# Kernel tuning notes

Measured on AMD Instinct MI355X. Metric: run time of the kernel, lower is better.

The kernel has to match this reference:

```python
import jax, jax.numpy as jnp
import numpy as np

B, S, D, H, HD = 4, 2048, 1024, 16, 64
R, L = 4, 256
MASKED_BIAS = -10000.0


def setup_inputs() -> dict:
    key = jax.random.key(0)
    ks = jax.random.split(key, 8)
    w = 0.02  # GPT-2 style init scale keeps softmax logits sane
    return {
        "hidden_states": jax.random.normal(ks[0], (B, S, D), jnp.float32),
        "latent": jax.random.normal(ks[1], (B, L), jnp.float32),
        "c_attn_w": jax.random.normal(ks[2], (D, 3 * D), jnp.float32) * w,
        "c_attn_b": jnp.zeros((3 * D,), jnp.float32),
        "c_proj_w": jax.random.normal(ks[3], (D, D), jnp.float32) * w,
        "c_proj_b": jnp.zeros((D,), jnp.float32),
        "text_w": jax.random.normal(ks[4], (R, D + 1, D), jnp.float32) * w,
        "text_b": jnp.zeros((R, D), jnp.float32),
        "lat_w": jax.random.normal(ks[5], (R, L + 1, D), jnp.float32) * w,
        "lat_b": jnp.zeros((R, D), jnp.float32),
    }


def _lmf(v, latent, text_w, text_b, lat_w, lat_b):
    # append bias-1 column, apply rank-R linears, sum over rank, outer-fuse
    b, s, _ = v.shape
    v1 = jnp.concatenate([v, jnp.ones((b, s, 1), v.dtype)], axis=-1)          # [B,S,D+1]
    l1 = jnp.concatenate([latent, jnp.ones((b, 1), latent.dtype)], axis=-1)   # [B,L+1]
    text_fusion = jnp.einsum("bsi,rio->bso", v1, text_w) + text_b.sum(0)      # [B,S,D]
    latent_fusion = jnp.einsum("bi,rio->bo", l1, lat_w) + lat_b.sum(0)        # [B,D]
    return text_fusion * latent_fusion[:, None, :]


def reference(hidden_states, latent, c_attn_w, c_attn_b, c_proj_w, c_proj_b,
              text_w, text_b, lat_w, lat_b):
    qkv = hidden_states @ c_attn_w + c_attn_b                # [B,S,3D] (Conv1D)
    q, k, v = jnp.split(qkv, 3, axis=-1)
    v = _lmf(v, latent, text_w, text_b, lat_w, lat_b)        # LMF on value stream

    def split_heads(t):
        return t.reshape(B, S, H, HD).transpose(0, 2, 1, 3)  # [B,H,S,HD]

    q, k, v = split_heads(q), split_heads(k), split_heads(v)
    scores = jnp.einsum("bhqd,bhkd->bhqk", q, k) / jnp.asarray(HD, q.dtype) ** 0.5
    causal = jnp.tril(jnp.ones((S, S), bool))                # use_causal_mask=True
    scores = jnp.where(causal, scores, jnp.asarray(MASKED_BIAS, scores.dtype))
    probs = jax.nn.softmax(scores, axis=-1)                  # attn_pdrop=0 (eval)
    attn = jnp.einsum("bhqk,bhkd->bhqd", probs, v)
    attn = attn.transpose(0, 2, 1, 3).reshape(B, S, D)       # merge heads
    return attn @ c_proj_w + c_proj_b                        # resid_pdrop=0 (eval)
```

## Files before the change

kernel.cpp:

```cpp
#include <hip/hip_runtime.h>
#include <hip/hip_bf16.h>

typedef __bf16 bf16;
typedef __bf16 bf16x8 __attribute__((ext_vector_type(8)));
typedef float f32x4 __attribute__((ext_vector_type(4)));
typedef unsigned short u16;
typedef unsigned int u32;

__device__ __forceinline__ u16 f2bf_bits(float f) {
    union { float f; u32 u; } v;
    v.f = f;
    u32 r = v.u + 0x7FFFu + ((v.u >> 16) & 1u);
    return (u16)(r >> 16);
}

__device__ __forceinline__ u32 pack_bf2(float a, float b) {
    union { __bf16 h[2]; u32 u; } v;
    v.h[0] = (__bf16)a;
    v.h[1] = (__bf16)b;
    return v.u;
}

__device__ __forceinline__ void gload_lds16(const void* g, void* l) {
    __builtin_amdgcn_global_load_lds((const __attribute__((address_space(1))) void*)g,
                                     (__attribute__((address_space(3))) void*)l, 16, 0, 0);
}


__global__ __launch_bounds__(256) void cvt_bf16_kernel(const float* __restrict__ in,
                                                       u32* __restrict__ out, int n4) {
    int i = blockIdx.x * 256 + threadIdx.x;
    if (i < n4) {
        float4 v = reinterpret_cast<const float4*>(in)[i];
        u32 lo = (u32)f2bf_bits(v.x) | ((u32)f2bf_bits(v.y) << 16);
        u32 hi = (u32)f2bf_bits(v.z) | ((u32)f2bf_bits(v.w) << 16);
        reinterpret_cast<uint2*>(out)[i] = make_uint2(lo, hi);
    }
}

__global__ __launch_bounds__(256) void transpose_sum_bf16(const float* __restrict__ in,
                                                          u16* __restrict__ out,
                                                          int K, int N, int R, long slab) {
    __shared__ float tile[32][33];
    int x = threadIdx.x & 31, ty = threadIdx.x >> 5;
    int k0 = blockIdx.y * 32, n0 = blockIdx.x * 32;
    for (int yy = ty; yy < 32; yy += 8) {
        float s = 0.f;
        for (int r = 0; r < R; ++r)
            s += in[(size_t)r * slab + (size_t)(k0 + yy) * N + n0 + x];
        tile[yy][x] = s;
    }
    __syncthreads();
    for (int yy = ty; yy < 32; yy += 8)
        out[(size_t)(n0 + yy) * K + k0 + x] = f2bf_bits(tile[x][yy]);
}

__global__ __launch_bounds__(256) void btfull_kernel(const float* __restrict__ tw,
                                                     const float* __restrict__ tb,
                                                     float* __restrict__ bt) {
    int o = blockIdx.x * 256 + threadIdx.x;
    float s = 0.f;
    for (int r = 0; r < 4; ++r)
        s += tw[(size_t)r * 1025 * 1024 + (size_t)1024 * 1024 + o] + tb[r * 1024 + o];
    bt[o] = s;
}

__global__ __launch_bounds__(256) void latw_sum_kernel(const float* __restrict__ lw,
                                                       float* __restrict__ wsum) {
    int i = blockIdx.x * 256 + threadIdx.x;
    if (i < 257 * 1024) {
        float s = 0.f;
        for (int r = 0; r < 4; ++r) s += lw[(size_t)r * 257 * 1024 + i];
        wsum[i] = s;
    }
}

__global__ __launch_bounds__(256) void latfuse_kernel(const float* __restrict__ latent,
                                                      const float* __restrict__ wsum,
                                                      const float* __restrict__ lb,
                                                      float* __restrict__ lf) {
    __shared__ float lat[256];
    const int b = blockIdx.y;
    const int o = blockIdx.x * 256 + threadIdx.x;
    lat[threadIdx.x] = latent[b * 256 + threadIdx.x];
    __syncthreads();
    float acc = wsum[(size_t)256 * 1024 + o];
    for (int r = 0; r < 4; ++r) acc += lb[r * 1024 + o];
#pragma unroll 8
    for (int i = 0; i < 256; ++i) acc += lat[i] * wsum[(size_t)i * 1024 + o];
    lf[b * 1024 + o] = acc;
}

template <int EPI>
__global__ __launch_bounds__(256) void gemm_bt(const bf16* __restrict__ A, int lda,
                                               const bf16* __restrict__ BT, int ldb,
                                               void* __restrict__ Cout, int ldc, int K,
                                               const float* __restrict__ bias,
                                               const float* __restrict__ scale) {
    __shared__ __align__(16) char As[16384];
    __shared__ __align__(16) char Bs[16384];
    const int tid = threadIdx.x;
    const int w = tid >> 6, l = tid & 63;

    const int nwgx = gridDim.x;
    const int nwg = nwgx * gridDim.y;
    const int wgid = blockIdx.y * nwgx + blockIdx.x;
    const int swz = (wgid & 7) * (nwg >> 3) + (wgid >> 3);
    const int m0 = (swz / nwgx) * 128, n0 = (swz % nwgx) * 128;
    const int wr = (w >> 1) * 64, wc = (w & 1) * 64;

    f32x4 acc[4][4] = {};
    const int kIters = K >> 6;

    const int srow = tid >> 3;
    const int scol = (tid & 7) * 8;
    const size_t aBase = (size_t)(m0 + srow) * lda + scol;
    const size_t bBase = (size_t)(n0 + srow) * ldb + scol;
    char* AsW = As + w * 1024;
    char* BsW = Bs + w * 1024;

    for (int kt = 0; kt < kIters; ++kt) {
        const int kk = kt << 6;
#pragma unroll
        for (int i = 0; i < 4; ++i) {
            gload_lds16(A + aBase + (size_t)(i * 32) * lda + kk, AsW + i * 4096);
            gload_lds16(BT + bBase + (size_t)(i * 32) * ldb + kk, BsW + i * 4096);
        }
        __syncthreads();
#pragma unroll
        for (int dc = 0; dc < 2; ++dc) {
            bf16x8 af[4], bfr[4];
#pragma unroll
            for (int m = 0; m < 4; ++m) {
                int off = (wr + m * 16 + (l & 15)) * 128 + dc * 64 + (l >> 4) * 16;
                af[m] = *reinterpret_cast<const bf16x8*>(As + off);
            }
#pragma unroll
            for (int n = 0; n < 4; ++n) {
                int off = (wc + n * 16 + (l & 15)) * 128 + dc * 64 + (l >> 4) * 16;
                bfr[n] = *reinterpret_cast<const bf16x8*>(Bs + off);
            }
#pragma unroll
            for (int m = 0; m < 4; ++m)
#pragma unroll
                for (int n = 0; n < 4; ++n)
                    acc[m][n] = __builtin_amdgcn_mfma_f32_16x16x32_bf16(af[m], bfr[n], acc[m][n], 0, 0, 0);
        }
        __syncthreads();
    }

    const bool qtile = (EPI == 3) && (n0 < 1024);
#pragma unroll
    for (int m = 0; m < 4; ++m) {
#pragma unroll
        for (int n = 0; n < 4; ++n) {
#pragma unroll
            for (int r = 0; r < 4; ++r) {
                int grow = m0 + wr + m * 16 + (l >> 4) * 4 + r;
                int gcol = n0 + wc + n * 16 + (l & 15);
                float v = acc[m][n][r];
                if (EPI == 1 || EPI == 3) v += bias[gcol];
                if (EPI == 3 && qtile) v *= 0.18033688011f;
                if (EPI == 2) {
                    v += bias[grow];
                    v *= scale[((gcol >> 11) << 10) | grow];
                }
                if (EPI == 1)
                    reinterpret_cast<float*>(Cout)[(size_t)grow * ldc + gcol] = v;
                else
                    reinterpret_cast<u16*>(Cout)[(size_t)grow * ldc + gcol] = f2bf_bits(v);
            }
        }
    }
}

__global__ __launch_bounds__(256) void attn_kernel(const bf16* __restrict__ qkv,
                                                   const bf16* __restrict__ vfT,
                                                   u16* __restrict__ out) {
    __shared__ __align__(16) char Kl[2][8192];
    __shared__ __align__(16) char Vt[2][8192];
    const int tid = threadIdx.x, w = tid >> 6, l = tid & 63;
    const int bh = blockIdx.y, b = bh >> 4, h = bh & 15;

    const int srowL = (l >> 3);
    const int cs = ((l & 7) ^ srowL) * 8;

    for (int ph = 0; ph < 2; ++ph) {
        const int qt = ph ? (15 - blockIdx.x) : blockIdx.x;
        const int q0 = qt * 128;
        const size_t rowQ = (size_t)(b * 2048 + q0 + w * 32);

        bf16x8 qfr[2][2];
#pragma unroll
        for (int qf = 0; qf < 2; ++qf)
#pragma unroll
            for (int dc = 0; dc < 2; ++dc)
                qfr[qf][dc] = *reinterpret_cast<const bf16x8*>(
                    qkv + (rowQ + qf * 16 + (l & 15)) * 3072 + h * 64 + dc * 32 + (l >> 4) * 8);

        f32x4 oacc[2][4] = {};
        float mrun[2] = {-1e30f, -1e30f};
        float lrun[2] = {0.f, 0.f};
        const int nt = (q0 + 128) >> 6;
        const int qmaxw = q0 + w * 32 + 31;

        auto stage = [&](int t, int buf) {
            const size_t kvb = (size_t)(b * 2048 + t * 64);
#pragma unroll
            for (int i = 0; i < 2; ++i) {
                int r = w * 8 + i * 32 + srowL;
                gload_lds16(qkv + (kvb + r) * 3072 + 1024 + h * 64 + cs,
                            Kl[buf] + w * 1024 + i * 4096);
                gload_lds16(vfT + (size_t)(h * 64 + r) * 8192 + kvb + cs,
                            Vt[buf] + w * 1024 + i * 4096);
            }
        };

        __syncthreads();
        stage(0, 0);
        int cur = 0;
        for (int t = 0; t < nt; ++t) {
            __syncthreads();
            if (t + 1 < nt) stage(t + 1, cur ^ 1);
            const int kv0 = t * 64;
            if (kv0 <= qmaxw) {
                const char* Kb = Kl[cur];
                const char* Vb = Vt[cur];
                f32x4 sacc[4][2] = {};
#pragma unroll
                for (int dc = 0; dc < 2; ++dc) {
#pragma unroll
                    for (int kf = 0; kf < 4; ++kf) {
                        int row = kf * 16 + (l & 15);
                        int off = (row * 128 + dc * 64 + (l >> 4) * 16) ^ ((row & 7) << 4);
                        bf16x8 kfr = *reinterpret_cast<const bf16x8*>(Kb + off);
#pragma unroll
                        for (int qf = 0; qf < 2; ++qf)
                            sacc[kf][qf] = __builtin_amdgcn_mfma_f32_16x16x32_bf16(
                                kfr, qfr[qf][dc], sacc[kf][qf], 0, 0, 0);
                    }
                }
                const bool needMask = (kv0 + 63) > (q0 + w * 32);
                bf16x8 pa[2][2];
#pragma unroll
                for (int qf = 0; qf < 2; ++qf) {
                    int qg = q0 + w * 32 + qf * 16 + (l & 15);
                    float p[4][4];
                    float tmax = -1e30f;
#pragma unroll
                    for (int kf = 0; kf < 4; ++kf)
#pragma unroll
                        for (int r = 0; r < 4; ++r) {
                            float s = sacc[kf][qf][r];
                            if (needMask) {
                                int kvg = kv0 + kf * 16 + (l >> 4) * 4 + r;
                                if (kvg > qg) s = -1e30f;
                            }
                            p[kf][r] = s;
                            tmax = fmaxf(tmax, s);
                        }
                    tmax = fmaxf(tmax, __shfl_xor(tmax, 16));
                    tmax = fmaxf(tmax, __shfl_xor(tmax, 32));
                    if (!__all(tmax <= mrun[qf] + 8.f)) {
                        float mnew = fmaxf(mrun[qf], tmax);
                        float alpha = exp2f(mrun[qf] - mnew);
                        mrun[qf] = mnew;
                        lrun[qf] *= alpha;
#pragma unroll
                        for (int r = 0; r < 4; ++r) {
                            float al = __shfl(alpha, (l >> 4) * 4 + r);
#pragma unroll
                            for (int hf = 0; hf < 4; ++hf) oacc[qf][hf][r] *= al;
                        }
                    }
                    const float m = mrun[qf];
                    float rsum = 0.f;
#pragma unroll
                    for (int kf = 0; kf < 4; ++kf) {
                        float p0 = exp2f(p[kf][0] - m), p1 = exp2f(p[kf][1] - m);
                        float p2 = exp2f(p[kf][2] - m), p3 = exp2f(p[kf][3] - m);
                        p[kf][0] = p0; p[kf][1] = p1; p[kf][2] = p2; p[kf][3] = p3;
                        rsum += (p0 + p1) + (p2 + p3);
                    }
                    rsum += __shfl_xor(rsum, 16);
                    rsum += __shfl_xor(rsum, 32);
                    lrun[qf] += rsum;
                    u32 c[4][2];
#pragma unroll
                    for (int kf = 0; kf < 4; ++kf) {
                        c[kf][0] = pack_bf2(p[kf][0], p[kf][1]);
                        c[kf][1] = pack_bf2(p[kf][2], p[kf][3]);
                    }
#pragma unroll
                    for (int kc = 0; kc < 2; ++kc) {
                        u32 wlo[2], whi[2];
#pragma unroll
                        for (int hh = 0; hh < 2; ++hh) {
                            u32 oe = c[2 * kc][hh], oo = c[2 * kc + 1][hh];
                            u32 xoe = (u32)__shfl_xor((int)oe, 32);
                            u32 xoo = (u32)__shfl_xor((int)oo, 32);
                            u32 P1 = (l & 32) ? xoo : oe;
                            u32 P2 = (l & 32) ? oo : xoe;
                            u32 z = (l & 16) ? P1 : P2;
                            u32 xz = (u32)__shfl_xor((int)z, 16);
                            wlo[hh] = (l & 16) ? xz : P1;
                            whi[hh] = (l & 16) ? P2 : xz;
                        }
                        union { u32 u[4]; bf16x8 v; } pv;
                        pv.u[0] = wlo[0]; pv.u[1] = wlo[1];
                        pv.u[2] = whi[0]; pv.u[3] = whi[1];
                        pa[qf][kc] = pv.v;
                    }
                }
#pragma unroll
                for (int kc = 0; kc < 2; ++kc) {
#pragma unroll
                    for (int hf = 0; hf < 4; ++hf) {
                        int hd = hf * 16 + (l & 15);
                        int off = (hd * 128 + kc * 64 + (l >> 4) * 16) ^ ((hd & 7) << 4);
                        bf16x8 vb = *reinterpret_cast<const bf16x8*>(Vb + off);
#pragma unroll
                        for (int qf = 0; qf < 2; ++qf)
                            oacc[qf][hf] = __builtin_amdgcn_mfma_f32_16x16x32_bf16(
                                pa[qf][kc], vb, oacc[qf][hf], 0, 0, 0);
                    }
                }
            }
            cur ^= 1;
        }

#pragma unroll
        for (int qf = 0; qf < 2; ++qf) {
#pragma unroll
            for (int r = 0; r < 4; ++r) {
                float linv = 1.0f / __shfl(lrun[qf], (l >> 4) * 4 + r);
                size_t grow = rowQ + qf * 16 + (l >> 4) * 4 + r;
#pragma unroll
                for (int hf = 0; hf < 4; ++hf)
                    out[grow * 1024 + h * 64 + hf * 16 + (l & 15)] =
                        f2bf_bits(oacc[qf][hf][r] * linv);
            }
        }
    }
}


extern "C" void kernel_launch(void* const* d_in, const int* in_sizes, int n_in,
                              void* d_out, int out_size, void* d_ws, size_t ws_size,
                              hipStream_t stream) {
    const float* hs     = (const float*)d_in[0];
    const float* latent = (const float*)d_in[1];
    const float* attnw  = (const float*)d_in[2];
    const float* attnb  = (const float*)d_in[3];
    const float* projw  = (const float*)d_in[4];
    const float* projb  = (const float*)d_in[5];
    const float* textw  = (const float*)d_in[6];
    const float* textb  = (const float*)d_in[7];
    const float* latw   = (const float*)d_in[8];
    const float* latb   = (const float*)d_in[9];

    char* ws = (char*)d_ws;
    size_t off = 0;
    auto alloc = [&](size_t bytes) {
        char* p = ws + off;
        off += (bytes + 255) & ~(size_t)255;
        return p;
    };
    u16* qkv    = (u16*)alloc((size_t)8192 * 3072 * 2);
    u16* hsbf   = (u16*)alloc((size_t)8192 * 1024 * 2);
    u16* vfT    = (u16*)alloc((size_t)1024 * 8192 * 2);
    u16* attnWT = (u16*)alloc((size_t)3072 * 1024 * 2);
    u16* projWT = (u16*)alloc((size_t)1024 * 1024 * 2);
    u16* WtT    = (u16*)alloc((size_t)1024 * 1024 * 2);
    float* btf  = (float*)alloc(1024 * 4);
    float* lf   = (float*)alloc(4 * 1024 * 4);
    float* wsum = (float*)alloc((size_t)257 * 1024 * 4);

    cvt_bf16_kernel<<<8192, 256, 0, stream>>>(hs, (u32*)hsbf, 8192 * 1024 / 4);
    transpose_sum_bf16<<<dim3(96, 32), 256, 0, stream>>>(attnw, attnWT, 1024, 3072, 1, 0);
    transpose_sum_bf16<<<dim3(32, 32), 256, 0, stream>>>(projw, projWT, 1024, 1024, 1, 0);
    transpose_sum_bf16<<<dim3(32, 32), 256, 0, stream>>>(textw, WtT, 1024, 1024, 4, (long)1025 * 1024);
    btfull_kernel<<<4, 256, 0, stream>>>(textw, textb, btf);
    latw_sum_kernel<<<1028, 256, 0, stream>>>(latw, wsum);
    latfuse_kernel<<<dim3(4, 4), 256, 0, stream>>>(latent, wsum, latb, lf);

    gemm_bt<3><<<dim3(24, 64), 256, 0, stream>>>(
        (const bf16*)hsbf, 1024, (const bf16*)attnWT, 1024, qkv, 3072, 1024, attnb, nullptr);
    gemm_bt<2><<<dim3(64, 8), 256, 0, stream>>>(
        (const bf16*)WtT, 1024, (const bf16*)qkv + 2048, 3072, vfT, 8192, 1024, btf, lf);
    attn_kernel<<<dim3(8, 64), 256, 0, stream>>>((const bf16*)qkv, (const bf16*)vfT, hsbf);
    gemm_bt<1><<<dim3(8, 64), 256, 0, stream>>>(
        (const bf16*)hsbf, 1024, (const bf16*)projWT, 1024, d_out, 1024, 1024, projb, nullptr);
}
```

Baseline: 408.0 us.

## Shrink attention query tile to 64 rows and add MFMA priority hints

The attention kernel's query tile drops from 128 to 64 rows per block, so each wave owns one 16-row fragment and the grid doubles to 16x64 blocks, still paired front/back for causal balance. The per-wave skip of fully masked KV tiles is removed because the tile now ends exactly at the diagonal. s_setprio brackets around the MFMA loops give those waves scheduling priority. This adds parallelism and cuts register use, but each K/V tile loaded into LDS is now reused by half as many query rows, raising K/V traffic.

```diff
diff --git a/kernel.cpp b/kernel.cpp
--- a/kernel.cpp
+++ b/kernel.cpp
@@ -186,23 +186,20 @@
     const int cs = ((l & 7) ^ srowL) * 8;
 
     for (int ph = 0; ph < 2; ++ph) {
-        const int qt = ph ? (15 - blockIdx.x) : blockIdx.x;
-        const int q0 = qt * 128;
-        const size_t rowQ = (size_t)(b * 2048 + q0 + w * 32);
-
-        bf16x8 qfr[2][2];
-#pragma unroll
-        for (int qf = 0; qf < 2; ++qf)
-#pragma unroll
-            for (int dc = 0; dc < 2; ++dc)
-                qfr[qf][dc] = *reinterpret_cast<const bf16x8*>(
-                    qkv + (rowQ + qf * 16 + (l & 15)) * 3072 + h * 64 + dc * 32 + (l >> 4) * 8);
-
-        f32x4 oacc[2][4] = {};
-        float mrun[2] = {-1e30f, -1e30f};
-        float lrun[2] = {0.f, 0.f};
-        const int nt = (q0 + 128) >> 6;
-        const int qmaxw = q0 + w * 32 + 31;
+        const int qt = ph ? (31 - blockIdx.x) : blockIdx.x;
+        const int q0 = qt * 64;
+        const size_t rowQ = (size_t)(b * 2048 + q0 + w * 16);
+
+        bf16x8 qfr[2];
+#pragma unroll
+        for (int dc = 0; dc < 2; ++dc)
+            qfr[dc] = *reinterpret_cast<const bf16x8*>(
+                qkv + (rowQ + (l & 15)) * 3072 + h * 64 + dc * 32 + (l >> 4) * 8);
+
+        f32x4 oacc[4] = {};
+        float mrun = -1e30f;
+        float lrun = 0.f;
+        const int nt = qt + 1;
 
         auto stage = [&](int t, int buf) {
             const size_t kvb = (size_t)(b * 2048 + t * 64);
@@ -223,123 +220,115 @@
             __syncthreads();
             if (t + 1 < nt) stage(t + 1, cur ^ 1);
             const int kv0 = t * 64;
-            if (kv0 <= qmaxw) {
-                const char* Kb = Kl[cur];
-                const char* Vb = Vt[cur];
-                f32x4 sacc[4][2] = {};
-#pragma unroll
-                for (int dc = 0; dc < 2; ++dc) {
-#pragma unroll
-                    for (int kf = 0; kf < 4; ++kf) {
-                        int row = kf * 16 + (l & 15);
-                        int off = (row * 128 + dc * 64 + (l >> 4) * 16) ^ ((row & 7) << 4);
-                        bf16x8 kfr = *reinterpret_cast<const bf16x8*>(Kb + off);
-#pragma unroll
-                        for (int qf = 0; qf < 2; ++qf)
-                            sacc[kf][qf] = __builtin_amdgcn_mfma_f32_16x16x32_bf16(
-                                kfr, qfr[qf][dc], sacc[kf][qf], 0, 0, 0);
+            const char* Kb = Kl[cur];
+            const char* Vb = Vt[cur];
+            f32x4 sacc[4] = {};
+            __builtin_amdgcn_s_setprio(1);
+#pragma unroll
+            for (int dc = 0; dc < 2; ++dc) {
+#pragma unroll
+                for (int kf = 0; kf < 4; ++kf) {
+                    int row = kf * 16 + (l & 15);
+                    int off = (row * 128 + dc * 64 + (l >> 4) * 16) ^ ((row & 7) << 4);
+                    bf16x8 kfr = *reinterpret_cast<const bf16x8*>(Kb + off);
+                    sacc[kf] = __builtin_amdgcn_mfma_f32_16x16x32_bf16(
+                        kfr, qfr[dc], sacc[kf], 0, 0, 0);
+                }
+            }
+            __builtin_amdgcn_s_setprio(0);
+            const bool needMask = (kv0 + 63) > (q0 + w * 16);
+            const int qg = q0 + w * 16 + (l & 15);
+            float p[4][4];
+            float tmax = -1e30f;
+#pragma unroll
+            for (int kf = 0; kf < 4; ++kf)
+#pragma unroll
+                for (int r = 0; r < 4; ++r) {
+                    float s = sacc[kf][r];
+                    if (needMask) {
+                        int kvg = kv0 + kf * 16 + (l >> 4) * 4 + r;
+                        if (kvg > qg) s = -1e30f;
                     }
-                }
-                const bool needMask = (kv0 + 63) > (q0 + w * 32);
-                bf16x8 pa[2][2];
-#pragma unroll
-                for (int qf = 0; qf < 2; ++qf) {
-                    int qg = q0 + w * 32 + qf * 16 + (l & 15);
-                    float p[4][4];
-                    float tmax = -1e30f;
-#pragma unroll
-                    for (int kf = 0; kf < 4; ++kf)
-#pragma unroll
-                        for (int r = 0; r < 4; ++r) {
-                            float s = sacc[kf][qf][r];
-                            if (needMask) {
-                                int kvg = kv0 + kf * 16 + (l >> 4) * 4 + r;
-                                if (kvg > qg) s = -1e30f;
-                            }
-                            p[kf][r] = s;
-                            tmax = fmaxf(tmax, s);
-                        }
-                    tmax = fmaxf(tmax, __shfl_xor(tmax, 16));
-                    tmax = fmaxf(tmax, __shfl_xor(tmax, 32));
-                    if (!__all(tmax <= mrun[qf] + 8.f)) {
-                        float mnew = fmaxf(mrun[qf], tmax);
-                        float alpha = exp2f(mrun[qf] - mnew);
-                        mrun[qf] = mnew;
-                        lrun[qf] *= alpha;
-#pragma unroll
-                        for (int r = 0; r < 4; ++r) {
-                            float al = __shfl(alpha, (l >> 4) * 4 + r);
-#pragma unroll
-                            for (int hf = 0; hf < 4; ++hf) oacc[qf][hf][r] *= al;
-                        }
-                    }
-                    const float m = mrun[qf];
-                    float rsum = 0.f;
-#pragma unroll
-                    for (int kf = 0; kf < 4; ++kf) {
-                        float p0 = exp2f(p[kf][0] - m), p1 = exp2f(p[kf][1] - m);
-                        float p2 = exp2f(p[kf][2] - m), p3 = exp2f(p[kf][3] - m);
-                        p[kf][0] = p0; p[kf][1] = p1; p[kf][2] = p2; p[kf][3] = p3;
-                        rsum += (p0 + p1) + (p2 + p3);
-                    }
-                    rsum += __shfl_xor(rsum, 16);
-                    rsum += __shfl_xor(rsum, 32);
-                    lrun[qf] += rsum;
-                    u32 c[4][2];
-#pragma unroll
-                    for (int kf = 0; kf < 4; ++kf) {
-                        c[kf][0] = pack_bf2(p[kf][0], p[kf][1]);
-                        c[kf][1] = pack_bf2(p[kf][2], p[kf][3]);
-                    }
-#pragma unroll
-                    for (int kc = 0; kc < 2; ++kc) {
-                        u32 wlo[2], whi[2];
-#pragma unroll
-                        for (int hh = 0; hh < 2; ++hh) {
-                            u32 oe = c[2 * kc][hh], oo = c[2 * kc + 1][hh];
-                            u32 xoe = (u32)__shfl_xor((int)oe, 32);
-                            u32 xoo = (u32)__shfl_xor((int)oo, 32);
-                            u32 P1 = (l & 32) ? xoo : oe;
-                            u32 P2 = (l & 32) ? oo : xoe;
-                            u32 z = (l & 16) ? P1 : P2;
-                            u32 xz = (u32)__shfl_xor((int)z, 16);
-                            wlo[hh] = (l & 16) ? xz : P1;
-                            whi[hh] = (l & 16) ? P2 : xz;
-                        }
-                        union { u32 u[4]; bf16x8 v; } pv;
-                        pv.u[0] = wlo[0]; pv.u[1] = wlo[1];
-                        pv.u[2] = whi[0]; pv.u[3] = whi[1];
-                        pa[qf][kc] = pv.v;
-                    }
-                }
-#pragma unroll
-                for (int kc = 0; kc < 2; ++kc) {
-#pragma unroll
-                    for (int hf = 0; hf < 4; ++hf) {
-                        int hd = hf * 16 + (l & 15);
-                        int off = (hd * 128 + kc * 64 + (l >> 4) * 16) ^ ((hd & 7) << 4);
-                        bf16x8 vb = *reinterpret_cast<const bf16x8*>(Vb + off);
-#pragma unroll
-                        for (int qf = 0; qf < 2; ++qf)
-                            oacc[qf][hf] = __builtin_amdgcn_mfma_f32_16x16x32_bf16(
-                                pa[qf][kc], vb, oacc[qf][hf], 0, 0, 0);
-                    }
-                }
-            }
+                    p[kf][r] = s;
+                    tmax = fmaxf(tmax, s);
+                }
+            tmax = fmaxf(tmax, __shfl_xor(tmax, 16));
+            tmax = fmaxf(tmax, __shfl_xor(tmax, 32));
+            if (!__all(tmax <= mrun + 8.f)) {
+                float mnew = fmaxf(mrun, tmax);
+                float alpha = exp2f(mrun - mnew);
+                mrun = mnew;
+                lrun *= alpha;
+#pragma unroll
+                for (int r = 0; r < 4; ++r) {
+                    float al = __shfl(alpha, (l >> 4) * 4 + r);
+#pragma unroll
+                    for (int hf = 0; hf < 4; ++hf) oacc[hf][r] *= al;
+                }
+            }
+            const float m = mrun;
+            float rsum = 0.f;
+#pragma unroll
+            for (int kf = 0; kf < 4; ++kf) {
+                float p0 = exp2f(p[kf][0] - m), p1 = exp2f(p[kf][1] - m);
+                float p2 = exp2f(p[kf][2] - m), p3 = exp2f(p[kf][3] - m);
+                p[kf][0] = p0; p[kf][1] = p1; p[kf][2] = p2; p[kf][3] = p3;
+                rsum += (p0 + p1) + (p2 + p3);
+            }
+            rsum += __shfl_xor(rsum, 16);
+            rsum += __shfl_xor(rsum, 32);
+            lrun += rsum;
+            u32 c[4][2];
+#pragma unroll
+            for (int kf = 0; kf < 4; ++kf) {
+                c[kf][0] = pack_bf2(p[kf][0], p[kf][1]);
+                c[kf][1] = pack_bf2(p[kf][2], p[kf][3]);
+            }
+            bf16x8 pa[2];
+#pragma unroll
+            for (int kc = 0; kc < 2; ++kc) {
+                u32 wlo[2], whi[2];
+#pragma unroll
+                for (int hh = 0; hh < 2; ++hh) {
+                    u32 oe = c[2 * kc][hh], oo = c[2 * kc + 1][hh];
+                    u32 xoe = (u32)__shfl_xor((int)oe, 32);
+                    u32 xoo = (u32)__shfl_xor((int)oo, 32);
+                    u32 P1 = (l & 32) ? xoo : oe;
+                    u32 P2 = (l & 32) ? oo : xoe;
+                    u32 z = (l & 16) ? P1 : P2;
+                    u32 xz = (u32)__shfl_xor((int)z, 16);
+                    wlo[hh] = (l & 16) ? xz : P1;
+                    whi[hh] = (l & 16) ? P2 : xz;
+                }
+                union { u32 u[4]; bf16x8 v; } pv;
+                pv.u[0] = wlo[0]; pv.u[1] = wlo[1];
+                pv.u[2] = whi[0]; pv.u[3] = whi[1];
+                pa[kc] = pv.v;
+            }
+            __builtin_amdgcn_s_setprio(1);
+#pragma unroll
+            for (int kc = 0; kc < 2; ++kc) {
+#pragma unroll
+                for (int hf = 0; hf < 4; ++hf) {
+                    int hd = hf * 16 + (l & 15);
+                    int off = (hd * 128 + kc * 64 + (l >> 4) * 16) ^ ((hd & 7) << 4);
+                    bf16x8 vb = *reinterpret_cast<const bf16x8*>(Vb + off);
+                    oacc[hf] = __builtin_amdgcn_mfma_f32_16x16x32_bf16(
+                        pa[kc], vb, oacc[hf], 0, 0, 0);
+                }
+            }
+            __builtin_amdgcn_s_setprio(0);
             cur ^= 1;
         }
 
 #pragma unroll
-        for (int qf = 0; qf < 2; ++qf) {
-#pragma unroll
-            for (int r = 0; r < 4; ++r) {
-                float linv = 1.0f / __shfl(lrun[qf], (l >> 4) * 4 + r);
-                size_t grow = rowQ + qf * 16 + (l >> 4) * 4 + r;
-#pragma unroll
-                for (int hf = 0; hf < 4; ++hf)
-                    out[grow * 1024 + h * 64 + hf * 16 + (l & 15)] =
-                        f2bf_bits(oacc[qf][hf][r] * linv);
-            }
+        for (int r = 0; r < 4; ++r) {
+            float linv = 1.0f / __shfl(lrun, (l >> 4) * 4 + r);
+            size_t grow = rowQ + (l >> 4) * 4 + r;
+#pragma unroll
+            for (int hf = 0; hf < 4; ++hf)
+                out[grow * 1024 + h * 64 + hf * 16 + (l & 15)] =
+                    f2bf_bits(oacc[hf][r] * linv);
         }
     }
 }
@@ -388,7 +377,7 @@
         (const bf16*)hsbf, 1024, (const bf16*)attnWT, 1024, qkv, 3072, 1024, attnb, nullptr);
     gemm_bt<2><<<dim3(64, 8), 256, 0, stream>>>(
         (const bf16*)WtT, 1024, (const bf16*)qkv + 2048, 3072, vfT, 8192, 1024, btf, lf);
-    attn_kernel<<<dim3(8, 64), 256, 0, stream>>>((const bf16*)qkv, (const bf16*)vfT, hsbf);
+    attn_kernel<<<dim3(16, 64), 256, 0, stream>>>((const bf16*)qkv, (const bf16*)vfT, hsbf);
     gemm_bt<1><<<dim3(8, 64), 256, 0, stream>>>(
         (const bf16*)hsbf, 1024, (const bf16*)projWT, 1024, d_out, 1024, 1024, projb, nullptr);
 }
```

After: 423.7 us. 1.04x slower.
